# Kernel tuning notes

Measured on AMD Instinct MI355X. Metric: run time of the kernel, lower is better.

## Reference

```python
import jax, jax.numpy as jnp
import numpy as np

D = 512          # d_model
DS = 32          # d_state
EXPAND = 2
HEADDIM = 64
R = 4            # mimo_rank
DIN = EXPAND * D             # 1024 inner dim
H = DIN // HEADDIM           # 16 heads
DFF = ((int(D * 8 / 3) + 7) // 8) * 8  # 1368 SwiGLU hidden
CHUNK = max(1, 64 // R)      # 16
BATCH, SEQ = 4, 512


def setup_inputs() -> dict:
    key = jax.random.key(0)
    ks = jax.random.split(key, 12)
    def w(k, shape, fan):
        return jax.random.normal(k, shape, jnp.float32) / np.float32(np.sqrt(fan))
    return {
        "x": jax.random.normal(ks[0], (BATCH, SEQ, D), jnp.float32),
        "mask": jnp.ones((BATCH, SEQ), jnp.float32),
        "norm1_w": jnp.ones((D,), jnp.float32),
        "norm2_w": jnp.ones((D,), jnp.float32),
        "Wz": w(ks[1], (D, DIN), D),
        "Wx": w(ks[2], (D, DIN), D),
        "Wb": w(ks[3], (D, H * R * DS), D),
        "Wc": w(ks[4], (D, H * R * DS), D),
        "Wdt": w(ks[5], (D, H), D),
        "dt_bias": jnp.zeros((H,), jnp.float32),
        "A_log": jnp.log(jnp.arange(1, H + 1, dtype=jnp.float32)),
        "D_skip": jnp.ones((H,), jnp.float32),
        "Wout": w(ks[6], (DIN, D), DIN),
        "w1": w(ks[7], (D, DFF), D),
        "w2": w(ks[8], (DFF, D), DFF),
        "w3": w(ks[9], (D, DFF), D),
    }


def rmsnorm(x, wgt, eps=1e-6):
    rms = jnp.sqrt(jnp.mean(x * x, axis=-1, keepdims=True) + eps)
    return x / rms * wgt


def ssm_mixer(x, Wz, Wx, Wb, Wc, Wdt, dt_bias, A_log, D_skip, Wout):
    # x: [B, S, D] (already masked)
    B, S, _ = x.shape
    pad = (CHUNK - S % CHUNK) % CHUNK
    if pad > 0:
        x = jnp.pad(x, ((0, 0), (0, pad), (0, 0)))
    Sp = x.shape[1]
    z = x @ Wz                                        # [B,Sp,DIN] gate
    u = (x @ Wx).reshape(B, Sp, H, HEADDIM)           # [B,Sp,H,P]
    Bm = (x @ Wb).reshape(B, Sp, H, R, DS)            # [B,Sp,H,R,N]
    Cm = (x @ Wc).reshape(B, Sp, H, R, DS)
    dt = jax.nn.softplus(x @ Wdt + dt_bias)           # [B,Sp,H]
    a = jnp.exp(dt * (-jnp.exp(A_log)))               # per-step decay [B,Sp,H]
    ud = u * dt[..., None]                            # discretized input

    def step(h, inp):
        a_t, B_t, C_t, ud_t = inp                     # [B,H], [B,H,R,N], [B,H,R,N], [B,H,P]
        h = a_t[:, :, None, None, None] * h + jnp.einsum('bhrn,bhp->bhrnp', B_t, ud_t)
        y = jnp.einsum('bhrn,bhrnp->bhp', C_t, h)
        return h, y

    h0 = jnp.zeros((B, H, R, DS, HEADDIM), x.dtype)
    xs = (a.swapaxes(0, 1), Bm.swapaxes(0, 1), Cm.swapaxes(0, 1), ud.swapaxes(0, 1))
    _, ys = jax.lax.scan(step, h0, xs)                # ys: [Sp,B,H,P]
    y = ys.swapaxes(0, 1) + u * D_skip[None, None, :, None]
    y = y.reshape(B, Sp, DIN) * jax.nn.silu(z)
    y = y @ Wout                                      # [B,Sp,D]
    return y[:, :S]


def reference(x, mask, norm1_w, norm2_w, Wz, Wx, Wb, Wc, Wdt, dt_bias,
              A_log, D_skip, Wout, w1, w2, w3):
    m = mask[..., None]
    xn = rmsnorm(x, norm1_w) * m
    y = ssm_mixer(xn, Wz, Wx, Wb, Wc, Wdt, dt_bias, A_log, D_skip, Wout) * m
    x = x + y
    xn2 = rmsnorm(x, norm2_w)
    x = x + (jax.nn.silu(xn2 @ w1) * (xn2 @ w3)) @ w2
    return x * m
```

## Files before the change

kernel.cpp:

```cpp
#include <hip/hip_runtime.h>
#include <hip/hip_bf16.h>
#include <math.h>

#define Bn 4
#define Sn 512
#define Dn 512
#define DINn 1024
#define Hn 16
#define Pn 64
#define RNn 128
#define DFFn 1368
#define KP2 1408
#define BSn (Bn*Sn)
#define CH 64
#define NCH (Sn/CH)
#define PSTR 6144
#define FPAD 2816
#define NSCAN (Bn*NCH*Hn)
#define NRMS 512

typedef __attribute__((ext_vector_type(8))) short short8;
typedef __attribute__((ext_vector_type(4))) float f32x4;
typedef __attribute__((ext_vector_type(4))) short short4v;

static __device__ __forceinline__ float bf2f(__hip_bfloat16 v){return __bfloat162float(v);}
static __device__ __forceinline__ __hip_bfloat16 f2bf(float v){return __float2bfloat16(v);}
static __device__ __forceinline__ short f2bfs(float v){ __hip_bfloat16 b=f2bf(v); short s; __builtin_memcpy(&s,&b,2); return s; }
static __device__ __forceinline__ float bfs2f(short s){ __hip_bfloat16 b; __builtin_memcpy(&b,&s,2); return bf2f(b); }

static __device__ __forceinline__ int xcd_swz(int bid, int q) {
  return (bid & 7) * q + (bid >> 3);
}

typedef const __attribute__((address_space(1))) unsigned int* gas1_u32p;
typedef __attribute__((address_space(3))) unsigned int* gas3_u32p;
static __device__ __forceinline__ void gl_lds16(const void* g, void* l) {
  __builtin_amdgcn_global_load_lds((gas1_u32p)g, (gas3_u32p)l, 16, 0, 0);
}

struct T8 {
  const float* src[8];
  const float* svec[8];
  __hip_bfloat16* dst[8];
  int Rr[8], Cc[8], RrPad[8], CcPad[8], gw[8];
  int start[9];
};

static __device__ __forceinline__ void transpose_tile(const T8& d, int bid, int t,
                                                      float (*tile)[65]) {
  int i = 0;
#pragma unroll
  for (int k = 1; k < 8; ++k) if (bid >= d.start[k]) i = k;
  int rel = bid - d.start[i];
  int gx = rel % d.gw[i], gy = rel / d.gw[i];
  const float* in = d.src[i];
  const float* sv = d.svec[i];
  __hip_bfloat16* out = d.dst[i];
  int Rr = d.Rr[i], Cc = d.Cc[i], RrPad = d.RrPad[i], CcPad = d.CcPad[i];
  int tx = t & 15, ty = t >> 4;
#pragma unroll
  for (int i4 = 0; i4 < 4; ++i4) {
    int r = gy * 64 + ty + i4 * 16;
    int c0 = gx * 64 + tx * 4;
    f32x4 v = (f32x4){0.f, 0.f, 0.f, 0.f};
    if (r < Rr && c0 + 3 < Cc) v = *(const f32x4*)(in + (size_t)r * Cc + c0);
    tile[ty + i4 * 16][tx * 4 + 0] = v[0];
    tile[ty + i4 * 16][tx * 4 + 1] = v[1];
    tile[ty + i4 * 16][tx * 4 + 2] = v[2];
    tile[ty + i4 * 16][tx * 4 + 3] = v[3];
  }
  __syncthreads();
#pragma unroll
  for (int i4 = 0; i4 < 4; ++i4) {
    int r2 = gx * 64 + ty + i4 * 16;
    int c2 = gy * 64 + tx * 4;
    if (r2 < CcPad && c2 + 3 < RrPad) {
      int k = ty + i4 * 16;
      float s0 = sv ? sv[c2 + 0] : 1.f;
      float s1 = sv ? sv[c2 + 1] : 1.f;
      float s2 = sv ? sv[c2 + 2] : 1.f;
      float s3 = sv ? sv[c2 + 3] : 1.f;
      short4v o;
      o.x = f2bfs(tile[tx * 4 + 0][k] * s0);
      o.y = f2bfs(tile[tx * 4 + 1][k] * s1);
      o.z = f2bfs(tile[tx * 4 + 2][k] * s2);
      o.w = f2bfs(tile[tx * 4 + 3][k] * s3);
      *(short4v*)((short*)out + (size_t)r2 * RrPad + c2) = o;
    }
  }
}

__global__ __launch_bounds__(256) void prep_kernel(
    T8 d, const float* __restrict__ x, const float* __restrict__ w,
    const float* __restrict__ mask, const float* __restrict__ Wdt,
    const float* __restrict__ dtb, const float* __restrict__ Alog,
    __hip_bfloat16* __restrict__ outb, float* __restrict__ dt,
    float* __restrict__ la, float* __restrict__ rs, int tstart) {
  __shared__ __align__(16) char smem[40960];
  int bid = blockIdx.x, t = threadIdx.x;
  if (bid < tstart) {
    transpose_tile(d, bid, t, (float(*)[65])smem);
  } else if (bid - tstart < NRMS) {
    float* wdtS = (float*)smem;
    float* xsS  = (float*)(smem + 32768);
#pragma unroll
    for (int i = 0; i < 8; ++i) {
      int idx = t + i * 256;
      *(f32x4*)&wdtS[idx * 4] = *(const f32x4*)&Wdt[idx * 4];
    }
    __syncthreads();
    int wv = t >> 6, lane = t & 63;
    int row = (bid - tstart) * 4 + wv;
    const float* xr = x + (size_t)row * Dn;
    f32x4 v0 = *(const f32x4*)(xr + lane * 4);
    f32x4 v1 = *(const f32x4*)(xr + 256 + lane * 4);
    float ss = v0[0]*v0[0] + v0[1]*v0[1] + v0[2]*v0[2] + v0[3]*v0[3]
             + v1[0]*v1[0] + v1[1]*v1[1] + v1[2]*v1[2] + v1[3]*v1[3];
#pragma unroll
    for (int o = 32; o > 0; o >>= 1) ss += __shfl_xor(ss, o);
    float sc = rsqrtf(ss * (1.f / Dn) + 1e-6f) * mask[row];
    f32x4 w0 = *(const f32x4*)(w + lane * 4);
    f32x4 w1 = *(const f32x4*)(w + 256 + lane * 4);
    f32x4 o0, o1;
#pragma unroll
    for (int j = 0; j < 4; ++j) { o0[j] = v0[j] * sc * w0[j]; o1[j] = v1[j] * sc * w1[j]; }
    short4v b0, b1;
    b0.x = f2bfs(o0[0]); b0.y = f2bfs(o0[1]); b0.z = f2bfs(o0[2]); b0.w = f2bfs(o0[3]);
    b1.x = f2bfs(o1[0]); b1.y = f2bfs(o1[1]); b1.z = f2bfs(o1[2]); b1.w = f2bfs(o1[3]);
    *(short4v*)((short*)outb + (size_t)row * Dn + lane * 4) = b0;
    *(short4v*)((short*)outb + (size_t)row * Dn + 256 + lane * 4) = b1;
    *(f32x4*)&xsS[wv * 512 + lane * 4] = o0;
    *(f32x4*)&xsS[wv * 512 + 256 + lane * 4] = o1;
    int h = lane >> 2, j = lane & 3;
    float s = 0.f;
#pragma unroll 8
    for (int kk = 0; kk < 128; ++kk) {
      int k = j + kk * 4;
      s = fmaf(xsS[wv * 512 + k], wdtS[k * Hn + h], s);
    }
    s += __shfl_down(s, 2, 4);
    s += __shfl_down(s, 1, 4);
    if (j == 0) {
      float v = s + dtb[h];
      float sp = (v > 20.f) ? v : log1pf(expf(v));
      float Ah = expf(Alog[h]);
      dt[(size_t)row * Hn + h] = sp;
      la[(size_t)row * Hn + h] = -Ah * sp;
    }
  } else {
    *(f32x4*)&rs[t * 8]     = (f32x4){0.f, 0.f, 0.f, 0.f};
    *(f32x4*)&rs[t * 8 + 4] = (f32x4){0.f, 0.f, 0.f, 0.f};
  }
}

__global__ __launch_bounds__(256) void gemm_kernel(
    const __hip_bfloat16* __restrict__ A, const __hip_bfloat16* __restrict__ BT,
    __hip_bfloat16* __restrict__ C, int M, int N, int K) {
  __shared__ short As[2][4096];
  __shared__ short Bs[2][4096];
  int mblocks = M >> 7;
  int wg = xcd_swz(blockIdx.x, (int)gridDim.x >> 3);
  int m0 = (wg % mblocks) * 128, n0 = (wg / mblocks) * 128;
  int t = threadIdx.x;
  int lane = t & 63, wv = t >> 6;
  int wm = (wv & 1) * 64, wn = (wv >> 1) * 64;
  f32x4 acc[4][4];
#pragma unroll
  for (int i = 0; i < 4; ++i)
#pragma unroll
    for (int j = 0; j < 4; ++j) acc[i][j] = (f32x4){0.f, 0.f, 0.f, 0.f};
  const short* Ag = (const short*)A;
  const short* Bg = (const short*)BT;
  int r0 = t >> 2, p = t & 3;
  int q0 = (p - (r0 >> 1)) & 3;
  int r1 = r0 + 64;
  int q1 = (p - (r1 >> 1)) & 3;
  const short* Asrc0 = Ag + (size_t)(m0 + r0) * K + 8 * q0;
  const short* Asrc1 = Ag + (size_t)(m0 + r1) * K + 8 * q1;
  const short* Bsrc0 = Bg + (size_t)(n0 + r0) * K + 8 * q0;
  const short* Bsrc1 = Bg + (size_t)(n0 + r1) * K + 8 * q1;
  int fr = lane & 15, fq = lane >> 4;
  int kTiles = K >> 5;
  auto stage = [&](int buf, int k0) {
    gl_lds16(Asrc0 + k0, &As[buf][wv * 512]);
    gl_lds16(Asrc1 + k0, &As[buf][2048 + wv * 512]);
    gl_lds16(Bsrc0 + k0, &Bs[buf][wv * 512]);
    gl_lds16(Bsrc1 + k0, &Bs[buf][2048 + wv * 512]);
  };
  auto domfma = [&](int buf) {
    short8 af[4], bfr[4];
#pragma unroll
    for (int i = 0; i < 4; ++i) {
      int rr = wm + i * 16 + fr;
      af[i] = *(const short8*)&As[buf][rr * 32 + (((rr >> 1) + fq) & 3) * 8];
    }
#pragma unroll
    for (int i = 0; i < 4; ++i) {
      int rr = wn + i * 16 + fr;
      bfr[i] = *(const short8*)&Bs[buf][rr * 32 + (((rr >> 1) + fq) & 3) * 8];
    }
#pragma unroll
    for (int mi = 0; mi < 4; ++mi)
#pragma unroll
      for (int ni = 0; ni < 4; ++ni)
        acc[mi][ni] = __builtin_amdgcn_mfma_f32_16x16x32_bf16(af[mi], bfr[ni], acc[mi][ni], 0, 0, 0);
  };
  stage(0, 0);
  for (int kt = 0; kt < kTiles; ++kt) {
    int buf = kt & 1;
    __syncthreads();
    if (kt + 1 < kTiles) stage(buf ^ 1, (kt + 1) << 5);
    domfma(buf);
  }
  int fq4 = (lane >> 4) * 4;
#pragma unroll
  for (int mi = 0; mi < 4; ++mi)
#pragma unroll
    for (int ni = 0; ni < 4; ++ni) {
      int col = n0 + wn + ni * 16 + fr;
      if (col < N) {
        int rowb = m0 + wm + mi * 16 + fq4;
#pragma unroll
        for (int r = 0; r < 4; ++r)
          C[(size_t)(rowb + r) * N + col] = f2bf(acc[mi][ni][r]);
      }
    }
}

template <int MODE>
__global__ __launch_bounds__(256) void gemm64_ep_kernel(
    const __hip_bfloat16* __restrict__ A, const __hip_bfloat16* __restrict__ BT,
    const float* __restrict__ aux, const float* __restrict__ mask,
    float* __restrict__ out, __hip_bfloat16* __restrict__ outb,
    float* __restrict__ rs, int M, int N, int K) {
  __shared__ short As[2][64][72];
  __shared__ short Bs[2][64][72];
  int mblocks = M >> 6;
  int wg = xcd_swz(blockIdx.x, (int)gridDim.x >> 3);
  int m0 = (wg % mblocks) * 64, n0 = (wg / mblocks) * 64;
  int t = threadIdx.x;
  int lane = t & 63, wv = t >> 6;
  int wm = (wv & 1) * 32, wn = (wv >> 1) * 32;
  f32x4 acc[2][2];
#pragma unroll
  for (int i = 0; i < 2; ++i)
#pragma unroll
    for (int j = 0; j < 2; ++j) acc[i][j] = (f32x4){0.f, 0.f, 0.f, 0.f};
  const short* Ag = (const short*)A;
  const short* Bg = (const short*)BT;
  int sr = t >> 2;
  int sc = (t & 3) * 16;
  const short* Ap = Ag + (size_t)(m0 + sr) * K + sc;
  const short* Bp = Bg + (size_t)(n0 + sr) * K + sc;
  int fr = lane & 15, fq = (lane >> 4) * 8;
  int kTiles = K >> 6;
  short8 a0A = 0, a1A = 0, b0A = 0, b1A = 0;
  short8 a0B = 0, a1B = 0, b0B = 0, b1B = 0;
  auto loadA = [&](int k0) {
    a0A = *(const short8*)(Ap + k0);
    a1A = *(const short8*)(Ap + k0 + 8);
    b0A = *(const short8*)(Bp + k0);
    b1A = *(const short8*)(Bp + k0 + 8);
  };
  auto loadB = [&](int k0) {
    a0B = *(const short8*)(Ap + k0);
    a1B = *(const short8*)(Ap + k0 + 8);
    b0B = *(const short8*)(Bp + k0);
    b1B = *(const short8*)(Bp + k0 + 8);
  };
  auto storeA = [&](int buf) {
    *(short8*)&As[buf][sr][sc] = a0A;
    *(short8*)&As[buf][sr][sc + 8] = a1A;
    *(short8*)&Bs[buf][sr][sc] = b0A;
    *(short8*)&Bs[buf][sr][sc + 8] = b1A;
  };
  auto storeB = [&](int buf) {
    *(short8*)&As[buf][sr][sc] = a0B;
    *(short8*)&As[buf][sr][sc + 8] = a1B;
    *(short8*)&Bs[buf][sr][sc] = b0B;
    *(short8*)&Bs[buf][sr][sc + 8] = b1B;
  };
  auto mfma = [&](int buf) {
#pragma unroll
    for (int kk = 0; kk < 2; ++kk) {
      short8 af[2], bfr[2];
#pragma unroll
      for (int i = 0; i < 2; ++i) af[i] = *(const short8*)&As[buf][wm + i * 16 + fr][kk * 32 + fq];
#pragma unroll
      for (int i = 0; i < 2; ++i) bfr[i] = *(const short8*)&Bs[buf][wn + i * 16 + fr][kk * 32 + fq];
#pragma unroll
      for (int mi = 0; mi < 2; ++mi)
#pragma unroll
        for (int ni = 0; ni < 2; ++ni)
          acc[mi][ni] = __builtin_amdgcn_mfma_f32_16x16x32_bf16(af[mi], bfr[ni], acc[mi][ni], 0, 0, 0);
    }
  };
  loadA(0);
  storeA(0);
  loadA(64);
  __syncthreads();
  for (int kt = 0; kt < kTiles; kt += 2) {
    storeA(1);
    if (kt + 2 < kTiles) loadB((kt + 2) << 6);
    mfma(0);
    __syncthreads();
    if (kt + 2 < kTiles) storeB(0);
    if (kt + 3 < kTiles) loadA((kt + 3) << 6);
    mfma(1);
    __syncthreads();
  }
  int fq4 = (lane >> 4) * 4;
  float rsum[2][4];
#pragma unroll
  for (int mi = 0; mi < 2; ++mi)
#pragma unroll
    for (int r = 0; r < 4; ++r) rsum[mi][r] = 0.f;
#pragma unroll
  for (int mi = 0; mi < 2; ++mi)
#pragma unroll
    for (int ni = 0; ni < 2; ++ni) {
      int col = n0 + wn + ni * 16 + fr;
#pragma unroll
      for (int r = 0; r < 4; ++r) {
        int row = m0 + wm + mi * 16 + fq4 + r;
        float m = mask[row];
        size_t a = (size_t)row * N + col;
        float v = acc[mi][ni][r];
        if (MODE == 1) {
          float ov = aux[a] + v * m;
          out[a] = ov;
          outb[a] = f2bf(ov);
          rsum[mi][r] += ov * ov;
        } else {
          out[a] = (aux[a] + v) * m;
        }
      }
    }
  if (MODE == 1) {
#pragma unroll
    for (int mi = 0; mi < 2; ++mi)
#pragma unroll
      for (int r = 0; r < 4; ++r) {
        float s = rsum[mi][r];
#pragma unroll
        for (int o = 8; o > 0; o >>= 1) s += __shfl_xor(s, o);
        if ((lane & 15) == 0) {
          int row = m0 + wm + mi * 16 + fq4 + r;
          atomicAdd(&rs[row], s);
        }
      }
  }
}

__global__ __launch_bounds__(256) void gemm64g_kernel(
    const __hip_bfloat16* __restrict__ A, const float* __restrict__ rs,
    const __hip_bfloat16* __restrict__ BT, __hip_bfloat16* __restrict__ G,
    int M, int K) {
  __shared__ short As[2][64][72];
  __shared__ short B1s[2][64][72];
  __shared__ short B3s[2][64][72];
  __shared__ float ssc[64];
  int mblocks = M >> 6;
  int wg = xcd_swz(blockIdx.x, (int)gridDim.x >> 3);
  int m0 = (wg % mblocks) * 64, n0 = (wg / mblocks) * 64;
  int t = threadIdx.x;
  int lane = t & 63, wv = t >> 6;
  int wm = (wv & 1) * 32, wn = (wv >> 1) * 32;
  f32x4 acc1[2][2], acc3[2][2];
#pragma unroll
  for (int i = 0; i < 2; ++i)
#pragma unroll
    for (int j = 0; j < 2; ++j) {
      acc1[i][j] = (f32x4){0.f, 0.f, 0.f, 0.f};
      acc3[i][j] = (f32x4){0.f, 0.f, 0.f, 0.f};
    }
  const short* Ag = (const short*)A;
  const short* Bg = (const short*)BT;
  int sr = t >> 2;
  int sc = (t & 3) * 16;
  const short* Ap  = Ag + (size_t)(m0 + sr) * K + sc;
  const short* B1p = Bg + (size_t)(n0 + sr) * K + sc;
  const short* B3p = Bg + (size_t)(KP2 + n0 + sr) * K + sc;
  int fr = lane & 15, fq = (lane >> 4) * 8;
  int kTiles = K >> 6;
  if (t < 64) ssc[t] = rsqrtf(rs[m0 + t] * (1.f / Dn) + 1e-6f);
  short8 a0A = 0, a1A = 0, c0A = 0, c1A = 0, d0A = 0, d1A = 0;
  short8 a0B = 0, a1B = 0, c0B = 0, c1B = 0, d0B = 0, d1B = 0;
  auto loadA = [&](int k0) {
    a0A = *(const short8*)(Ap + k0);
    a1A = *(const short8*)(Ap + k0 + 8);
    c0A = *(const short8*)(B1p + k0);
    c1A = *(const short8*)(B1p + k0 + 8);
    d0A = *(const short8*)(B3p + k0);
    d1A = *(const short8*)(B3p + k0 + 8);
  };
  auto loadB = [&](int k0) {
    a0B = *(const short8*)(Ap + k0);
    a1B = *(const short8*)(Ap + k0 + 8);
    c0B = *(const short8*)(B1p + k0);
    c1B = *(const short8*)(B1p + k0 + 8);
    d0B = *(const short8*)(B3p + k0);
    d1B = *(const short8*)(B3p + k0 + 8);
  };
  auto storeA = [&](int buf) {
    *(short8*)&As[buf][sr][sc] = a0A;
    *(short8*)&As[buf][sr][sc + 8] = a1A;
    *(short8*)&B1s[buf][sr][sc] = c0A;
    *(short8*)&B1s[buf][sr][sc + 8] = c1A;
    *(short8*)&B3s[buf][sr][sc] = d0A;
    *(short8*)&B3s[buf][sr][sc + 8] = d1A;
  };
  auto storeB = [&](int buf) {
    *(short8*)&As[buf][sr][sc] = a0B;
    *(short8*)&As[buf][sr][sc + 8] = a1B;
    *(short8*)&B1s[buf][sr][sc] = c0B;
    *(short8*)&B1s[buf][sr][sc + 8] = c1B;
    *(short8*)&B3s[buf][sr][sc] = d0B;
    *(short8*)&B3s[buf][sr][sc + 8] = d1B;
  };
  auto mfma = [&](int buf) {
#pragma unroll
    for (int kk = 0; kk < 2; ++kk) {
      short8 af[2], b1f[2], b3f[2];
#pragma unroll
      for (int i = 0; i < 2; ++i) af[i]  = *(const short8*)&As[buf][wm + i * 16 + fr][kk * 32 + fq];
#pragma unroll
      for (int i = 0; i < 2; ++i) b1f[i] = *(const short8*)&B1s[buf][wn + i * 16 + fr][kk * 32 + fq];
#pragma unroll
      for (int i = 0; i < 2; ++i) b3f[i] = *(const short8*)&B3s[buf][wn + i * 16 + fr][kk * 32 + fq];
#pragma unroll
      for (int mi = 0; mi < 2; ++mi)
#pragma unroll
        for (int ni = 0; ni < 2; ++ni) {
          acc1[mi][ni] = __builtin_amdgcn_mfma_f32_16x16x32_bf16(af[mi], b1f[ni], acc1[mi][ni], 0, 0, 0);
          acc3[mi][ni] = __builtin_amdgcn_mfma_f32_16x16x32_bf16(af[mi], b3f[ni], acc3[mi][ni], 0, 0, 0);
        }
    }
  };
  loadA(0);
  storeA(0);
  loadA(64);
  __syncthreads();
  for (int kt = 0; kt < kTiles; kt += 2) {
    storeA(1);
    if (kt + 2 < kTiles) loadB((kt + 2) << 6);
    mfma(0);
    __syncthreads();
    if (kt + 2 < kTiles) storeB(0);
    if (kt + 3 < kTiles) loadA((kt + 3) << 6);
    mfma(1);
    __syncthreads();
  }
  int fq4 = (lane >> 4) * 4;
#pragma unroll
  for (int mi = 0; mi < 2; ++mi)
#pragma unroll
    for (int ni = 0; ni < 2; ++ni) {
      int col = n0 + wn + ni * 16 + fr;
#pragma unroll
      for (int r = 0; r < 4; ++r) {
        int rloc = wm + mi * 16 + fq4 + r;
        float scl = ssc[rloc];
        float h1v = acc1[mi][ni][r] * scl;
        float sil = h1v / (1.f + __expf(-h1v));
        float g = sil * (acc3[mi][ni][r] * scl);
        G[(size_t)(m0 + rloc) * KP2 + col] = f2bf(g);
      }
    }
}

__global__ __launch_bounds__(256) void chunk_intra_kernel(
    const __hip_bfloat16* __restrict__ P, const float* __restrict__ dt,
    const float* __restrict__ la, __hip_bfloat16* __restrict__ ysb,
    __hip_bfloat16* __restrict__ Sbuf, float* __restrict__ ecL, float* __restrict__ ec) {
  int id = blockIdx.x;
  int h = id & 15, c = (id >> 4) & 7, b = id >> 7;
  int t = threadIdx.x, lane = t & 63, wv = t >> 6;
  __shared__ __align__(16) char smem[55040];
  short* sCB = (short*)smem;
  short* sB  = (short*)(smem + 18432);
  short* sUD = (short*)(smem + 35840);
  short* sG  = (short*)(smem + 45056);
  float* scum = (float*)(smem + 54272);
  float* sws  = scum + 64;
  float* sdt  = sws + 64;
  int row0 = b * Sn + c * CH;
  const short* Pb = (const short*)P;
#pragma unroll
  for (int i = 0; i < 4; ++i) {
    int idx = t + i * 256;
    int r = idx >> 4, kk = (idx & 15) * 8;
    *(short8*)&sCB[r * 136 + kk] = *(const short8*)(Pb + (size_t)(row0 + r) * PSTR + 4096 + h * 128 + kk);
    *(short8*)&sB [r * 136 + kk] = *(const short8*)(Pb + (size_t)(row0 + r) * PSTR + 2048 + h * 128 + kk);
  }
  if (t < 64) { sdt[t] = dt[(size_t)(row0 + t) * Hn + h]; scum[t] = la[(size_t)(row0 + t) * Hn + h]; }
  __syncthreads();
  if (wv == 0) {
    float v = scum[lane];
#pragma unroll
    for (int o = 1; o < 64; o <<= 1) { float n = __shfl_up(v, o); if (lane >= o) v += n; }
    scum[lane] = v;
    float c63 = __shfl(v, 63);
    sws[lane] = __expf(c63 - v);
    ec[((size_t)((b * NCH + c) * Hn + h)) * 64 + lane] = __expf(v);
    if (lane == 0) ecL[(b * NCH + c) * Hn + h] = __expf(c63);
  }
#pragma unroll
  for (int i = 0; i < 2; ++i) {
    int idx = t + i * 256;
    int s = idx >> 3, pc = (idx & 7) * 8;
    short8 uv = *(const short8*)(Pb + (size_t)(row0 + s) * PSTR + 1024 + h * 64 + pc);
    float dv = sdt[s];
#pragma unroll
    for (int j = 0; j < 8; ++j) sUD[(pc + j) * 72 + s] = f2bfs(bfs2f(uv[j]) * dv);
  }
  __syncthreads();
  int fr = lane & 15, fq = (lane >> 4) * 8, q4 = (lane >> 4) * 4;
  {
    short8 af[4];
#pragma unroll
    for (int k = 0; k < 4; ++k) af[k] = *(short8*)&sCB[(16 * wv + fr) * 136 + k * 32 + fq];
#pragma unroll
    for (int j = 0; j < 4; ++j) {
      f32x4 acc = (f32x4){0.f, 0.f, 0.f, 0.f};
#pragma unroll
      for (int k = 0; k < 4; ++k) {
        short8 bf = *(short8*)&sB[(16 * j + fr) * 136 + k * 32 + fq];
        acc = __builtin_amdgcn_mfma_f32_16x16x32_bf16(af[k], bf, acc, 0, 0, 0);
      }
      int ss = 16 * j + fr;
      float cs = scum[ss];
#pragma unroll
      for (int r = 0; r < 4; ++r) {
        int tt = 16 * wv + q4 + r;
        float w = (ss <= tt) ? __expf(scum[tt] - cs) : 0.f;
        sG[tt * 72 + ss] = f2bfs(acc[r] * w);
      }
    }
  }
  __syncthreads();
#pragma unroll
  for (int i = 0; i < 32; ++i) {
    int idx = t + i * 256;
    int rn = idx >> 6, s = idx & 63;
    sCB[rn * 72 + s] = f2bfs(bfs2f(sB[s * 136 + rn]) * sws[s]);
  }
  __syncthreads();
  {
    short8 ag[2];
#pragma unroll
    for (int k = 0; k < 2; ++k) ag[k] = *(short8*)&sG[(16 * wv + fr) * 72 + k * 32 + fq];
#pragma unroll
    for (int j = 0; j < 4; ++j) {
      f32x4 acc = (f32x4){0.f, 0.f, 0.f, 0.f};
#pragma unroll
      for (int k = 0; k < 2; ++k) {
        short8 bf = *(short8*)&sUD[(16 * j + fr) * 72 + k * 32 + fq];
        acc = __builtin_amdgcn_mfma_f32_16x16x32_bf16(ag[k], bf, acc, 0, 0, 0);
      }
#pragma unroll
      for (int r = 0; r < 4; ++r)
        ysb[(size_t)(row0 + 16 * wv + q4 + r) * DINn + h * 64 + 16 * j + fr] = f2bf(acc[r]);
    }
  }
#pragma unroll
  for (int mt0 = 0; mt0 < 2; ++mt0) {
    int mt = wv * 2 + mt0;
    short8 ab[2];
#pragma unroll
    for (int k = 0; k < 2; ++k) ab[k] = *(short8*)&sCB[(16 * mt + fr) * 72 + k * 32 + fq];
#pragma unroll
    for (int j = 0; j < 4; ++j) {
      f32x4 acc = (f32x4){0.f, 0.f, 0.f, 0.f};
#pragma unroll
      for (int k = 0; k < 2; ++k) {
        short8 bf = *(short8*)&sUD[(16 * j + fr) * 72 + k * 32 + fq];
        acc = __builtin_amdgcn_mfma_f32_16x16x32_bf16(ab[k], bf, acc, 0, 0, 0);
      }
      int pp = 16 * j + fr;
      int rn0 = 16 * mt + q4;
      short4v o;
      o.x = f2bfs(acc[0]); o.y = f2bfs(acc[1]); o.z = f2bfs(acc[2]); o.w = f2bfs(acc[3]);
      *(short4v*)&((short*)Sbuf)[((size_t)((b * NCH + c) * Hn + h) * 64 + pp) * 128 + rn0] = o;
    }
  }
}

__global__ __launch_bounds__(256) void inter_gate_kernel(
    const __hip_bfloat16* __restrict__ P, const __hip_bfloat16* __restrict__ Sbuf,
    const float* __restrict__ ecL, const float* __restrict__ ec,
    const __hip_bfloat16* __restrict__ ysb, const float* __restrict__ Dsk,
    __hip_bfloat16* __restrict__ y2b) {
  int id = blockIdx.x;
  int h = id & 15, c = (id >> 4) & 7, b = id >> 7;
  int t = threadIdx.x, lane = t & 63, wv = t >> 6;
  __shared__ __align__(16) short sC[64 * 136];
  __shared__ __align__(16) short sHt[64 * 136];
  __shared__ __align__(16) short sz[64 * 64];
  __shared__ __align__(16) short su[64 * 64];
  __shared__ float sec[64];
  int row0 = b * Sn + c * CH;
  const short* Pb = (const short*)P;
#pragma unroll
  for (int i = 0; i < 2; ++i) {
    int idx = t + i * 256;
    int r = idx >> 3, pc = (idx & 7) * 8;
    *(short8*)&sz[r * 64 + pc] = *(const short8*)(Pb + (size_t)(row0 + r) * PSTR + h * 64 + pc);
    *(short8*)&su[r * 64 + pc] = *(const short8*)(Pb + (size_t)(row0 + r) * PSTR + 1024 + h * 64 + pc);
  }
  if (c > 0) {
#pragma unroll
    for (int i = 0; i < 4; ++i) {
      int idx = t + i * 256;
      int r = idx >> 4, kk = (idx & 15) * 8;
      *(short8*)&sC[r * 136 + kk] = *(const short8*)(Pb + (size_t)(row0 + r) * PSTR + 4096 + h * 128 + kk);
    }
    float hacc[32];
#pragma unroll
    for (int jj = 0; jj < 32; ++jj) hacc[jj] = 0.f;
    const short* Sb = (const short*)Sbuf;
    float wrun = 1.f;
    for (int cp = c - 1; cp >= 0; --cp) {
      size_t base = ((size_t)((b * NCH + cp) * Hn + h)) * 8192 + (size_t)t * 32;
#pragma unroll
      for (int v4 = 0; v4 < 4; ++v4) {
        short8 sv = *(const short8*)(Sb + base + v4 * 8);
#pragma unroll
        for (int jj = 0; jj < 8; ++jj)
          hacc[v4 * 8 + jj] = fmaf(wrun, bfs2f(sv[jj]), hacc[v4 * 8 + jj]);
      }
      wrun *= ecL[(size_t)((b * NCH + cp) * Hn + h)];
    }
    int p = t >> 2, rn0 = (t & 3) * 32;
#pragma unroll
    for (int v4 = 0; v4 < 4; ++v4) {
      short8 o;
#pragma unroll
      for (int jj = 0; jj < 8; ++jj) o[jj] = f2bfs(hacc[v4 * 8 + jj]);
      *(short8*)&sHt[p * 136 + rn0 + v4 * 8] = o;
    }
    if (t < 64) sec[t] = ec[((size_t)((b * NCH + c) * Hn + h)) * 64 + t];
  }
  __syncthreads();
  int fr = lane & 15, fq = (lane >> 4) * 8, q4 = (lane >> 4) * 4;
  f32x4 acc[4];
#pragma unroll
  for (int j = 0; j < 4; ++j) acc[j] = (f32x4){0.f, 0.f, 0.f, 0.f};
  if (c > 0) {
    short8 af[4];
#pragma unroll
    for (int k = 0; k < 4; ++k) af[k] = *(short8*)&sC[(16 * wv + fr) * 136 + k * 32 + fq];
#pragma unroll
    for (int j = 0; j < 4; ++j)
#pragma unroll
      for (int k = 0; k < 4; ++k) {
        short8 bf = *(short8*)&sHt[(16 * j + fr) * 136 + k * 32 + fq];
        acc[j] = __builtin_amdgcn_mfma_f32_16x16x32_bf16(af[k], bf, acc[j], 0, 0, 0);
      }
  }
  float dsk = Dsk[h];
#pragma unroll
  for (int j = 0; j < 4; ++j) {
    int col = 16 * j + fr;
#pragma unroll
    for (int r = 0; r < 4; ++r) {
      int tt = 16 * wv + q4 + r;
      size_t a = (size_t)(row0 + tt) * DINn + h * 64 + col;
      float val = bf2f(ysb[a]);
      if (c > 0) val += sec[tt] * acc[j][r];
      float uu = bfs2f(su[tt * 64 + col]);
      float zz = bfs2f(sz[tt * 64 + col]);
      float sil = zz / (1.f + __expf(-zz));
      y2b[a] = f2bf((val + uu * dsk) * sil);
    }
  }
}

extern "C" void kernel_launch(void* const* d_in, const int* in_sizes, int n_in,
                              void* d_out, int out_size, void* d_ws, size_t ws_size,
                              hipStream_t stream) {
  const float* x    = (const float*)d_in[0];
  const float* mask = (const float*)d_in[1];
  const float* n1w  = (const float*)d_in[2];
  const float* n2w  = (const float*)d_in[3];
  const float* Wz   = (const float*)d_in[4];
  const float* Wx   = (const float*)d_in[5];
  const float* Wb   = (const float*)d_in[6];
  const float* Wc   = (const float*)d_in[7];
  const float* Wdt  = (const float*)d_in[8];
  const float* dtb  = (const float*)d_in[9];
  const float* Alog = (const float*)d_in[10];
  const float* Dsk  = (const float*)d_in[11];
  const float* Wout = (const float*)d_in[12];
  const float* w1   = (const float*)d_in[13];
  const float* w2   = (const float*)d_in[14];
  const float* w3   = (const float*)d_in[15];

  char* ws = (char*)d_ws;
  size_t off = 0;
  auto alloc = [&](size_t bytes) {
    char* p = ws + off;
    off += (bytes + 255) & ~(size_t)255;
    return p;
  };
  __hip_bfloat16* xnb = (__hip_bfloat16*)alloc((size_t)BSn * Dn * 2);
  __hip_bfloat16* P = (__hip_bfloat16*)alloc((size_t)BSn * PSTR * 2);
  float* dt  = (float*)alloc((size_t)BSn * Hn * 4);
  float* la  = (float*)alloc((size_t)BSn * Hn * 4);
  __hip_bfloat16* ysb = (__hip_bfloat16*)alloc((size_t)BSn * DINn * 2);
  float* ecL = (float*)alloc((size_t)Bn * NCH * Hn * 4);
  float* ec  = (float*)alloc((size_t)Bn * NCH * Hn * 64 * 4);
  float* rs  = (float*)alloc((size_t)BSn * 4);
  __hip_bfloat16* WallT = (__hip_bfloat16*)alloc((size_t)PSTR * Dn * 2);
  __hip_bfloat16* WoutT = (__hip_bfloat16*)alloc((size_t)Dn * DINn * 2);
  __hip_bfloat16* w13T  = (__hip_bfloat16*)alloc((size_t)FPAD * Dn * 2);
  __hip_bfloat16* w2T   = (__hip_bfloat16*)alloc((size_t)Dn * KP2 * 2);
  char* arena = alloc(23200000);
  __hip_bfloat16* Sbuf = (__hip_bfloat16*)arena;
  __hip_bfloat16* y2b  = (__hip_bfloat16*)(arena + 16777216);
  float* xres          = (float*)arena;
  __hip_bfloat16* gatedb = (__hip_bfloat16*)(arena + 4194304);
  __hip_bfloat16* xresb  = (__hip_bfloat16*)(arena + 20971520);

  T8 td;
  for (int i = 0; i < 8; ++i) td.svec[i] = nullptr;
  td.src[0] = Wz;   td.dst[0] = WallT;                      td.Rr[0] = 512;  td.Cc[0] = 1024; td.RrPad[0] = 512;  td.CcPad[0] = 1024;
  td.src[1] = Wx;   td.dst[1] = WallT + (size_t)1024 * 512; td.Rr[1] = 512;  td.Cc[1] = 1024; td.RrPad[1] = 512;  td.CcPad[1] = 1024;
  td.src[2] = Wb;   td.dst[2] = WallT + (size_t)2048 * 512; td.Rr[2] = 512;  td.Cc[2] = 2048; td.RrPad[2] = 512;  td.CcPad[2] = 2048;
  td.src[3] = Wc;   td.dst[3] = WallT + (size_t)4096 * 512; td.Rr[3] = 512;  td.Cc[3] = 2048; td.RrPad[3] = 512;  td.CcPad[3] = 2048;
  td.src[4] = Wout; td.dst[4] = WoutT;                      td.Rr[4] = 1024; td.Cc[4] = 512;  td.RrPad[4] = 1024; td.CcPad[4] = 512;
  td.src[5] = w1;   td.dst[5] = w13T;                       td.Rr[5] = 512;  td.Cc[5] = 1368; td.RrPad[5] = 512;  td.CcPad[5] = KP2;
  td.src[6] = w3;   td.dst[6] = w13T + (size_t)KP2 * 512;   td.Rr[6] = 512;  td.Cc[6] = 1368; td.RrPad[6] = 512;  td.CcPad[6] = KP2;
  td.src[7] = w2;   td.dst[7] = w2T;                        td.Rr[7] = 1368; td.Cc[7] = 512;  td.RrPad[7] = KP2;  td.CcPad[7] = 512;
  td.svec[5] = n2w;
  td.svec[6] = n2w;
  int tot = 0;
  for (int i = 0; i < 8; ++i) {
    td.gw[i] = (td.CcPad[i] + 63) / 64;
    int gh = (td.RrPad[i] + 63) / 64;
    td.start[i] = tot;
    tot += td.gw[i] * gh;
  }
  td.start[8] = tot;

  prep_kernel<<<tot + NRMS + 1, 256, 0, stream>>>(td, x, n1w, mask, Wdt, dtb, Alog, xnb, dt, la, rs, tot);
  gemm_kernel<<<16 * 48, 256, 0, stream>>>(xnb, WallT, P, BSn, PSTR, Dn);
  chunk_intra_kernel<<<NSCAN, 256, 0, stream>>>(P, dt, la, ysb, Sbuf, ecL, ec);
  inter_gate_kernel<<<NSCAN, 256, 0, stream>>>(P, Sbuf, ecL, ec, ysb, Dsk, y2b);
  gemm64_ep_kernel<1><<<32 * 8, 256, 0, stream>>>(y2b, WoutT, x, mask, xres, xresb, rs, BSn, Dn, DINn);
  gemm64g_kernel<<<32 * (KP2 / 64), 256, 0, stream>>>(xresb, rs, w13T, gatedb, BSn, Dn);
  gemm64_ep_kernel<2><<<32 * 8, 256, 0, stream>>>(gatedb, w2T, xres, mask, (float*)d_out, nullptr, rs, BSn, Dn, KP2);
}
```

Baseline: 185.0 us.

## Move intra-chunk output computation into the inter-chunk gate kernel

Splits the SSM scan work differently. The first kernel now only computes chunk states and decay totals. The second kernel computes the intra-chunk C·B attention and its output in registers, then adds the inter-chunk contribution and applies the gate. This removes the global round-trip of the bf16 intra-chunk output and the per-step decay buffer, and it reuses the C tile already loaded in shared memory. In exchange the second kernel does more work and holds more registers while loading prior states.

```diff
diff --git a/kernel.cpp b/kernel.cpp
--- a/kernel.cpp
+++ b/kernel.cpp
@@ -469,21 +469,97 @@
     }
 }
 
-__global__ __launch_bounds__(256) void chunk_intra_kernel(
+__global__ __launch_bounds__(256) void chunk_state_kernel(
     const __hip_bfloat16* __restrict__ P, const float* __restrict__ dt,
-    const float* __restrict__ la, __hip_bfloat16* __restrict__ ysb,
-    __hip_bfloat16* __restrict__ Sbuf, float* __restrict__ ecL, float* __restrict__ ec) {
+    const float* __restrict__ la, __hip_bfloat16* __restrict__ Sbuf,
+    float* __restrict__ ecL) {
   int id = blockIdx.x;
   int h = id & 15, c = (id >> 4) & 7, b = id >> 7;
   int t = threadIdx.x, lane = t & 63, wv = t >> 6;
-  __shared__ __align__(16) char smem[55040];
-  short* sCB = (short*)smem;
-  short* sB  = (short*)(smem + 18432);
-  short* sUD = (short*)(smem + 35840);
-  short* sG  = (short*)(smem + 45056);
-  float* scum = (float*)(smem + 54272);
+  __shared__ __align__(16) char smem[45824];
+  short* sB   = (short*)smem;
+  short* sUD  = (short*)(smem + 17408);
+  short* sBwT = (short*)(smem + 26624);
+  float* scum = (float*)(smem + 45056);
   float* sws  = scum + 64;
   float* sdt  = sws + 64;
+  int row0 = b * Sn + c * CH;
+  const short* Pb = (const short*)P;
+#pragma unroll
+  for (int i = 0; i < 4; ++i) {
+    int idx = t + i * 256;
+    int r = idx >> 4, kk = (idx & 15) * 8;
+    *(short8*)&sB[r * 136 + kk] = *(const short8*)(Pb + (size_t)(row0 + r) * PSTR + 2048 + h * 128 + kk);
+  }
+  if (t < 64) { sdt[t] = dt[(size_t)(row0 + t) * Hn + h]; scum[t] = la[(size_t)(row0 + t) * Hn + h]; }
+  __syncthreads();
+  if (wv == 0) {
+    float v = scum[lane];
+#pragma unroll
+    for (int o = 1; o < 64; o <<= 1) { float n = __shfl_up(v, o); if (lane >= o) v += n; }
+    float c63 = __shfl(v, 63);
+    sws[lane] = __expf(c63 - v);
+    if (lane == 0) ecL[(b * NCH + c) * Hn + h] = __expf(c63);
+  }
+#pragma unroll
+  for (int i = 0; i < 2; ++i) {
+    int idx = t + i * 256;
+    int s = idx >> 3, pc = (idx & 7) * 8;
+    short8 uv = *(const short8*)(Pb + (size_t)(row0 + s) * PSTR + 1024 + h * 64 + pc);
+    float dv = sdt[s];
+#pragma unroll
+    for (int j = 0; j < 8; ++j) sUD[(pc + j) * 72 + s] = f2bfs(bfs2f(uv[j]) * dv);
+  }
+  __syncthreads();
+#pragma unroll
+  for (int i = 0; i < 32; ++i) {
+    int idx = t + i * 256;
+    int rn = idx >> 6, s = idx & 63;
+    sBwT[rn * 72 + s] = f2bfs(bfs2f(sB[s * 136 + rn]) * sws[s]);
+  }
+  __syncthreads();
+  int fr = lane & 15, fq = (lane >> 4) * 8, q4 = (lane >> 4) * 4;
+#pragma unroll
+  for (int mt0 = 0; mt0 < 2; ++mt0) {
+    int mt = wv * 2 + mt0;
+    short8 ab[2];
+#pragma unroll
+    for (int k = 0; k < 2; ++k) ab[k] = *(short8*)&sBwT[(16 * mt + fr) * 72 + k * 32 + fq];
+#pragma unroll
+    for (int j = 0; j < 4; ++j) {
+      f32x4 acc = (f32x4){0.f, 0.f, 0.f, 0.f};
+#pragma unroll
+      for (int k = 0; k < 2; ++k) {
+        short8 bf = *(short8*)&sUD[(16 * j + fr) * 72 + k * 32 + fq];
+        acc = __builtin_amdgcn_mfma_f32_16x16x32_bf16(ab[k], bf, acc, 0, 0, 0);
+      }
+      int pp = 16 * j + fr;
+      int rn0 = 16 * mt + q4;
+      short4v o;
+      o.x = f2bfs(acc[0]); o.y = f2bfs(acc[1]); o.z = f2bfs(acc[2]); o.w = f2bfs(acc[3]);
+      *(short4v*)&((short*)Sbuf)[((size_t)((b * NCH + c) * Hn + h) * 64 + pp) * 128 + rn0] = o;
+    }
+  }
+}
+
+__global__ __launch_bounds__(256) void intra_inter_gate_kernel(
+    const __hip_bfloat16* __restrict__ P, const float* __restrict__ dt,
+    const float* __restrict__ la, const __hip_bfloat16* __restrict__ Sbuf,
+    const float* __restrict__ ecL, const float* __restrict__ Dsk,
+    __hip_bfloat16* __restrict__ y2b) {
+  int id = blockIdx.x;
+  int h = id & 15, c = (id >> 4) & 7, b = id >> 7;
+  int t = threadIdx.x, lane = t & 63, wv = t >> 6;
+  __shared__ __align__(16) char smem[54016];
+  short* sCB = (short*)smem;
+  short* sB  = (short*)(smem + 17408);
+  short* sUD = (short*)(smem + 34816);
+  short* sG  = (short*)(smem + 44032);
+  short* sHt = (short*)(smem + 34816);
+  short* sz  = sB;
+  short* su  = sB + 4096;
+  float* scum = (float*)(smem + 53248);
+  float* sdt  = scum + 64;
   int row0 = b * Sn + c * CH;
   const short* Pb = (const short*)P;
 #pragma unroll
@@ -500,10 +576,6 @@
 #pragma unroll
     for (int o = 1; o < 64; o <<= 1) { float n = __shfl_up(v, o); if (lane >= o) v += n; }
     scum[lane] = v;
-    float c63 = __shfl(v, 63);
-    sws[lane] = __expf(c63 - v);
-    ec[((size_t)((b * NCH + c) * Hn + h)) * 64 + lane] = __expf(v);
-    if (lane == 0) ecL[(b * NCH + c) * Hn + h] = __expf(c63);
   }
 #pragma unroll
   for (int i = 0; i < 2; ++i) {
@@ -539,13 +611,7 @@
     }
   }
   __syncthreads();
-#pragma unroll
-  for (int i = 0; i < 32; ++i) {
-    int idx = t + i * 256;
-    int rn = idx >> 6, s = idx & 63;
-    sCB[rn * 72 + s] = f2bfs(bfs2f(sB[s * 136 + rn]) * sws[s]);
-  }
-  __syncthreads();
+  f32x4 ysr[4];
   {
     short8 ag[2];
 #pragma unroll
@@ -558,49 +624,9 @@
         short8 bf = *(short8*)&sUD[(16 * j + fr) * 72 + k * 32 + fq];
         acc = __builtin_amdgcn_mfma_f32_16x16x32_bf16(ag[k], bf, acc, 0, 0, 0);
       }
-#pragma unroll
-      for (int r = 0; r < 4; ++r)
-        ysb[(size_t)(row0 + 16 * wv + q4 + r) * DINn + h * 64 + 16 * j + fr] = f2bf(acc[r]);
-    }
-  }
-#pragma unroll
-  for (int mt0 = 0; mt0 < 2; ++mt0) {
-    int mt = wv * 2 + mt0;
-    short8 ab[2];
-#pragma unroll
-    for (int k = 0; k < 2; ++k) ab[k] = *(short8*)&sCB[(16 * mt + fr) * 72 + k * 32 + fq];
-#pragma unroll
-    for (int j = 0; j < 4; ++j) {
-      f32x4 acc = (f32x4){0.f, 0.f, 0.f, 0.f};
-#pragma unroll
-      for (int k = 0; k < 2; ++k) {
-        short8 bf = *(short8*)&sUD[(16 * j + fr) * 72 + k * 32 + fq];
-        acc = __builtin_amdgcn_mfma_f32_16x16x32_bf16(ab[k], bf, acc, 0, 0, 0);
-      }
-      int pp = 16 * j + fr;
-      int rn0 = 16 * mt + q4;
-      short4v o;
-      o.x = f2bfs(acc[0]); o.y = f2bfs(acc[1]); o.z = f2bfs(acc[2]); o.w = f2bfs(acc[3]);
-      *(short4v*)&((short*)Sbuf)[((size_t)((b * NCH + c) * Hn + h) * 64 + pp) * 128 + rn0] = o;
-    }
-  }
-}
-
-__global__ __launch_bounds__(256) void inter_gate_kernel(
-    const __hip_bfloat16* __restrict__ P, const __hip_bfloat16* __restrict__ Sbuf,
-    const float* __restrict__ ecL, const float* __restrict__ ec,
-    const __hip_bfloat16* __restrict__ ysb, const float* __restrict__ Dsk,
-    __hip_bfloat16* __restrict__ y2b) {
-  int id = blockIdx.x;
-  int h = id & 15, c = (id >> 4) & 7, b = id >> 7;
-  int t = threadIdx.x, lane = t & 63, wv = t >> 6;
-  __shared__ __align__(16) short sC[64 * 136];
-  __shared__ __align__(16) short sHt[64 * 136];
-  __shared__ __align__(16) short sz[64 * 64];
-  __shared__ __align__(16) short su[64 * 64];
-  __shared__ float sec[64];
-  int row0 = b * Sn + c * CH;
-  const short* Pb = (const short*)P;
+      ysr[j] = acc;
+    }
+  }
 #pragma unroll
   for (int i = 0; i < 2; ++i) {
     int idx = t + i * 256;
@@ -608,16 +634,10 @@
     *(short8*)&sz[r * 64 + pc] = *(const short8*)(Pb + (size_t)(row0 + r) * PSTR + h * 64 + pc);
     *(short8*)&su[r * 64 + pc] = *(const short8*)(Pb + (size_t)(row0 + r) * PSTR + 1024 + h * 64 + pc);
   }
+  float hacc[32];
+#pragma unroll
+  for (int jj = 0; jj < 32; ++jj) hacc[jj] = 0.f;
   if (c > 0) {
-#pragma unroll
-    for (int i = 0; i < 4; ++i) {
-      int idx = t + i * 256;
-      int r = idx >> 4, kk = (idx & 15) * 8;
-      *(short8*)&sC[r * 136 + kk] = *(const short8*)(Pb + (size_t)(row0 + r) * PSTR + 4096 + h * 128 + kk);
-    }
-    float hacc[32];
-#pragma unroll
-    for (int jj = 0; jj < 32; ++jj) hacc[jj] = 0.f;
     const short* Sb = (const short*)Sbuf;
     float wrun = 1.f;
     for (int cp = c - 1; cp >= 0; --cp) {
@@ -631,25 +651,26 @@
       }
       wrun *= ecL[(size_t)((b * NCH + cp) * Hn + h)];
     }
-    int p = t >> 2, rn0 = (t & 3) * 32;
+  }
+  __syncthreads();
+  if (c > 0) {
+    int pp = t >> 2, rn0 = (t & 3) * 32;
 #pragma unroll
     for (int v4 = 0; v4 < 4; ++v4) {
       short8 o;
 #pragma unroll
       for (int jj = 0; jj < 8; ++jj) o[jj] = f2bfs(hacc[v4 * 8 + jj]);
-      *(short8*)&sHt[p * 136 + rn0 + v4 * 8] = o;
-    }
-    if (t < 64) sec[t] = ec[((size_t)((b * NCH + c) * Hn + h)) * 64 + t];
-  }
-  __syncthreads();
-  int fr = lane & 15, fq = (lane >> 4) * 8, q4 = (lane >> 4) * 4;
+      *(short8*)&sHt[pp * 136 + rn0 + v4 * 8] = o;
+    }
+  }
+  __syncthreads();
   f32x4 acc[4];
 #pragma unroll
   for (int j = 0; j < 4; ++j) acc[j] = (f32x4){0.f, 0.f, 0.f, 0.f};
   if (c > 0) {
     short8 af[4];
 #pragma unroll
-    for (int k = 0; k < 4; ++k) af[k] = *(short8*)&sC[(16 * wv + fr) * 136 + k * 32 + fq];
+    for (int k = 0; k < 4; ++k) af[k] = *(short8*)&sCB[(16 * wv + fr) * 136 + k * 32 + fq];
 #pragma unroll
     for (int j = 0; j < 4; ++j)
 #pragma unroll
@@ -666,8 +687,8 @@
     for (int r = 0; r < 4; ++r) {
       int tt = 16 * wv + q4 + r;
       size_t a = (size_t)(row0 + tt) * DINn + h * 64 + col;
-      float val = bf2f(ysb[a]);
-      if (c > 0) val += sec[tt] * acc[j][r];
+      float val = ysr[j][r];
+      if (c > 0) val += __expf(scum[tt]) * acc[j][r];
       float uu = bfs2f(su[tt * 64 + col]);
       float zz = bfs2f(sz[tt * 64 + col]);
       float sil = zz / (1.f + __expf(-zz));
@@ -707,9 +728,7 @@
   __hip_bfloat16* P = (__hip_bfloat16*)alloc((size_t)BSn * PSTR * 2);
   float* dt  = (float*)alloc((size_t)BSn * Hn * 4);
   float* la  = (float*)alloc((size_t)BSn * Hn * 4);
-  __hip_bfloat16* ysb = (__hip_bfloat16*)alloc((size_t)BSn * DINn * 2);
   float* ecL = (float*)alloc((size_t)Bn * NCH * Hn * 4);
-  float* ec  = (float*)alloc((size_t)Bn * NCH * Hn * 64 * 4);
   float* rs  = (float*)alloc((size_t)BSn * 4);
   __hip_bfloat16* WallT = (__hip_bfloat16*)alloc((size_t)PSTR * Dn * 2);
   __hip_bfloat16* WoutT = (__hip_bfloat16*)alloc((size_t)Dn * DINn * 2);
@@ -745,8 +764,8 @@
 
   prep_kernel<<<tot + NRMS + 1, 256, 0, stream>>>(td, x, n1w, mask, Wdt, dtb, Alog, xnb, dt, la, rs, tot);
   gemm_kernel<<<16 * 48, 256, 0, stream>>>(xnb, WallT, P, BSn, PSTR, Dn);
-  chunk_intra_kernel<<<NSCAN, 256, 0, stream>>>(P, dt, la, ysb, Sbuf, ecL, ec);
-  inter_gate_kernel<<<NSCAN, 256, 0, stream>>>(P, Sbuf, ecL, ec, ysb, Dsk, y2b);
+  chunk_state_kernel<<<NSCAN, 256, 0, stream>>>(P, dt, la, Sbuf, ecL);
+  intra_inter_gate_kernel<<<NSCAN, 256, 0, stream>>>(P, dt, la, Sbuf, ecL, Dsk, y2b);
   gemm64_ep_kernel<1><<<32 * 8, 256, 0, stream>>>(y2b, WoutT, x, mask, xres, xresb, rs, BSn, Dn, DINn);
   gemm64g_kernel<<<32 * (KP2 / 64), 256, 0, stream>>>(xresb, rs, w13T, gatedb, BSn, Dn);
   gemm64_ep_kernel<2><<<32 * 8, 256, 0, stream>>>(gatedb, w2T, xres, mask, (float*)d_out, nullptr, rs, BSn, Dn, KP2);
```

Result: no change. 182.9 us (median of 2 runs) (-1.1%).
